# Kernel optimization log

Hardware: AMD Instinct MI355X
Metric: run time of the kernel (lower is better)

## Reference

```python
import jax, jax.numpy as jnp
import numpy as np

S, B, D, W = 2048, 4, 1024, 256  # seq_len, batch, d_model, local_window_size


def create_local_mask(seq_len, w):
    # Faithful to source: tril(w-1) then tril(-(w-1)) -> keeps j <= i-(w-1)
    m = jnp.ones((seq_len, seq_len), dtype=bool)
    m = jnp.tril(m, w - 1)
    m = jnp.tril(m, -(w - 1))
    return m


def setup_inputs() -> dict:
    key = jax.random.key(0)
    ks = jax.random.split(key, 12)
    w = lambda k: jax.random.normal(k, (D, D), dtype=jnp.float32) * 0.02
    return {
        "query": jax.random.normal(ks[0], (S, B, D), dtype=jnp.float32),
        "key_in": jax.random.normal(ks[1], (S, B, D), dtype=jnp.float32),
        "value": jax.random.normal(ks[2], (S, B, D), dtype=jnp.float32),
        "Wq": w(ks[3]), "bq": jnp.zeros((D,), jnp.float32),
        "Wk": w(ks[4]), "bk": jnp.zeros((D,), jnp.float32),
        "Wv": w(ks[5]), "bv": jnp.zeros((D,), jnp.float32),
        "pos_bias": jax.random.normal(ks[6], (S, S), dtype=jnp.float32) * 0.02,
        "Wo": w(ks[7]), "bo": jnp.zeros((D,), jnp.float32),
        "mask": jnp.ones((S, S, 1), dtype=bool),
    }


def reference(query, key_in, value, Wq, bq, Wk, bk, Wv, bv, pos_bias, Wo, bo, mask):
    # Linear projections (torch Linear: x @ W.T + b)
    q = jnp.einsum('sbd,ed->sbe', query, Wq) + bq
    k = jnp.einsum('sbd,ed->sbe', key_in, Wk) + bk
    v = jnp.einsum('sbd,ed->sbe', value, Wv) + bv

    local_mask = create_local_mask(S, W)
    pb = (pos_bias * local_mask.astype(pos_bias.dtype))[:, :, None]  # [S,S,1]
    pb = jnp.where(mask, pb, -jnp.inf)

    max_key = jnp.max(k, axis=0, keepdims=True)          # [1,B,D]
    max_pb = jnp.max(pb, axis=1, keepdims=True)          # [S,1,1]
    exp_key = jnp.exp(k - max_key)                       # [S,B,D]
    exp_pb = jnp.exp(pb - max_pb)                        # [S,S,B] after broadcast

    num = jnp.einsum('ijb,jbd->ibd', exp_pb, exp_key * v)
    den = jnp.einsum('ijb,jbd->ibd', exp_pb, exp_key)
    y = jax.nn.sigmoid(q) * num / den
    return jnp.einsum('sbd,ed->sbe', y, Wo) + bo
```

## Files before the change

kernel.cpp:

```cpp
#include <hip/hip_runtime.h>
#include <hip/hip_bf16.h>
#include <cstdint>


typedef short short8 __attribute__((ext_vector_type(8)));
typedef float f32x4 __attribute__((ext_vector_type(4)));

#define S_LEN 2048
#define NBD 4096
#define SBD 8388608
#define DD 1048576
#define SS 4194304

#define ASZ 8192
#define BUFSZ 24576
#define GASZ 4096
#define GBUF 12288
#define AS1 __attribute__((address_space(1)))
#define AS3 __attribute__((address_space(3)))

__device__ __forceinline__ unsigned short f2bf(float f) {
  union { float f; unsigned int u; } x; x.f = f;
  unsigned int u = x.u;
  unsigned int r = u + 0x7fffu + ((u >> 16) & 1u);
  return (unsigned short)(r >> 16);
}
__device__ __forceinline__ float bf2f(unsigned short b) {
  union { unsigned int u; float f; } x; x.u = ((unsigned int)b) << 16;
  return x.f;
}

__global__ __launch_bounds__(256) void k_cvt3(
    const float* __restrict__ a, const float* __restrict__ b, const float* __restrict__ c,
    unsigned short* __restrict__ oa, unsigned short* __restrict__ ob,
    unsigned short* __restrict__ oc) {
  const int w = blockIdx.x;
  const int arr = w >> 11;
  const int b2 = w & 2047;
  const float* src = arr == 0 ? a : (arr == 1 ? b : c);
  unsigned short* dst = arr == 0 ? oa : (arr == 1 ? ob : oc);
  const size_t t0 = (size_t)b2 * 256 + threadIdx.x;
#pragma unroll
  for (int it = 0; it < 2; ++it) {
    const size_t base = (t0 + (size_t)it * 524288) * 8;
    float4 x0 = *(const float4*)(src + base);
    float4 x1 = *(const float4*)(src + base + 4);
    short8 s;
    s[0] = (short)f2bf(x0.x); s[1] = (short)f2bf(x0.y);
    s[2] = (short)f2bf(x0.z); s[3] = (short)f2bf(x0.w);
    s[4] = (short)f2bf(x1.x); s[5] = (short)f2bf(x1.y);
    s[6] = (short)f2bf(x1.z); s[7] = (short)f2bf(x1.w);
    *(short8*)(dst + base) = s;
  }
}

__global__ void k_cvt4w(const float* __restrict__ wq, const float* __restrict__ wk,
                        const float* __restrict__ wv, const float* __restrict__ wo,
                        unsigned short* __restrict__ wcat, unsigned short* __restrict__ wob) {
  int i = (blockIdx.x * blockDim.x + threadIdx.x) * 4;
  float4 fq = *(const float4*)(wq + i);
  float4 fk = *(const float4*)(wk + i);
  float4 fv = *(const float4*)(wv + i);
  float4 fo = *(const float4*)(wo + i);
  ushort4 u;
  u.x = f2bf(fq.x); u.y = f2bf(fq.y); u.z = f2bf(fq.z); u.w = f2bf(fq.w);
  *(ushort4*)(wcat + i) = u;
  u.x = f2bf(fk.x); u.y = f2bf(fk.y); u.z = f2bf(fk.z); u.w = f2bf(fk.w);
  *(ushort4*)(wcat + DD + i) = u;
  u.x = f2bf(fv.x); u.y = f2bf(fv.y); u.z = f2bf(fv.z); u.w = f2bf(fv.w);
  *(ushort4*)(wcat + 2 * DD + i) = u;
  u.x = f2bf(fo.x); u.y = f2bf(fo.y); u.z = f2bf(fo.z); u.w = f2bf(fo.w);
  *(ushort4*)(wob + i) = u;
}

__global__ void k_build_c(const float* __restrict__ pb, unsigned short* __restrict__ C) {
  int i4 = (blockIdx.x * blockDim.x + threadIdx.x) * 4;
  float4 p = *(const float4*)(pb + i4);
  const int i = i4 >> 11;
  const int j = i4 & 2047;
  ushort4 o;
  o.x = f2bf((i >= j + 255) ? expm1f(p.x) : 0.0f);
  o.y = f2bf((i >= j + 256) ? expm1f(p.y) : 0.0f);
  o.z = f2bf((i >= j + 257) ? expm1f(p.z) : 0.0f);
  o.w = f2bf((i >= j + 258) ? expm1f(p.w) : 0.0f);
  *(ushort4*)(C + i4) = o;
}

__global__ __launch_bounds__(256) void k_eu_transpose(
    const unsigned short* __restrict__ kbf, const unsigned short* __restrict__ vbf,
    unsigned short* __restrict__ Mt, float* __restrict__ totals) {
  __shared__ unsigned short Lu[64][65];
  __shared__ unsigned short Le[64][65];
  const int n0 = blockIdx.x * 64;
  const int j0 = blockIdx.y * 64;
  const int t = threadIdx.x;
  const int c = t & 63;
  const int jq = t >> 6;
  float ptu = 0.f, pte = 0.f;
#pragma unroll 4
  for (int s = 0; s < 16; ++s) {
    int jj = jq + s * 4;
    size_t g = (size_t)(j0 + jj) * NBD + n0 + c;
    float kv = bf2f(kbf[g]);
    float vv = bf2f(vbf[g]);
    float e = __expf(kv);
    float u = e * vv;
    Le[jj][c] = f2bf(e);
    Lu[jj][c] = f2bf(u);
    pte += e; ptu += u;
  }
  atomicAdd(&totals[n0 + c], ptu);
  atomicAdd(&totals[NBD + n0 + c], pte);
  __syncthreads();
  const int jj2 = t & 63;
  const int nq = t >> 6;
#pragma unroll 4
  for (int s = 0; s < 16; ++s) {
    int nn = nq + s * 4;
    int ru = 2 * n0 + 32 * (nn >> 4) + (nn & 15);
    Mt[(size_t)ru * S_LEN + j0 + jj2] = Lu[jj2][nn];
    Mt[(size_t)(ru + 16) * S_LEN + j0 + jj2] = Le[jj2][nn];
  }
}

#define SBAR() do { __builtin_amdgcn_sched_barrier(0); __builtin_amdgcn_s_barrier(); \
                    __builtin_amdgcn_sched_barrier(0); } while (0)
#define VM(n)  do { asm volatile("s_waitcnt vmcnt(" #n ")" ::: "memory"); \
                    __builtin_amdgcn_sched_barrier(0); } while (0)
#define LGK0() do { asm volatile("s_waitcnt lgkmcnt(0)" ::: "memory"); \
                    __builtin_amdgcn_sched_barrier(0); } while (0)

#define G32_STAGE(tile, bidx) do {                                                        \
    const int k0_ = (tile) * 32;                                                          \
    __builtin_amdgcn_global_load_lds(                                                     \
        (const AS1 unsigned int*)(Ag + (size_t)(m0 + wave * 16 + lr4) * 1024 + k0_ + lc4),\
        (AS3 unsigned int*)&lds[(bidx) * GBUF + wave * 512 + lane * 8], 16, 0, 0);        \
    _Pragma("unroll") for (int q_ = 0; q_ < 2; ++q_) {                                    \
      const int g_ = wave * 2 + q_;                                                       \
      __builtin_amdgcn_global_load_lds(                                                   \
          (const AS1 unsigned int*)(Bg + (size_t)(n0 + g_ * 16 + lr4) * 1024 + k0_ + lc4),\
          (AS3 unsigned int*)&lds[(bidx) * GBUF + GASZ + g_ * 512 + lane * 8], 16, 0, 0); \
    }                                                                                     \
  } while (0)

#define G32_READF(RA, RB, bidx) do {                                                      \
    _Pragma("unroll") for (int f_ = 0; f_ < 4; ++f_)                                      \
      RA[f_] = *(const short8*)&lds[(bidx) * GBUF + (wr + f_ * 16 + l15) * 32 + swg];     \
    _Pragma("unroll") for (int f_ = 0; f_ < 4; ++f_)                                      \
      RB[f_] = *(const short8*)&lds[(bidx) * GBUF + GASZ + (wc + f_ * 16 + l15) * 32 + swg];\
  } while (0)

#define G32_MFMA(RA, RB) do {                                                             \
    __builtin_amdgcn_s_setprio(1);                                                        \
    _Pragma("unroll") for (int i_ = 0; i_ < 4; ++i_)                                      \
    _Pragma("unroll") for (int j_ = 0; j_ < 4; ++j_)                                      \
      acc[i_][j_] = __builtin_amdgcn_mfma_f32_16x16x32_bf16(RA[i_], RB[j_],               \
                                                            acc[i_][j_], 0, 0, 0);       \
    __builtin_amdgcn_s_setprio(0);                                                        \
  } while (0)

__global__ __launch_bounds__(512, 4) void k_qkv32(
    const unsigned short* __restrict__ A0, const unsigned short* __restrict__ A1,
    const unsigned short* __restrict__ A2, const unsigned short* __restrict__ Bg,
    const float* __restrict__ b0, const float* __restrict__ b1, const float* __restrict__ b2,
    unsigned short* __restrict__ o0, unsigned short* __restrict__ o1,
    unsigned short* __restrict__ o2) {
  __shared__ unsigned short lds[3 * GBUF];

  const int tid = threadIdx.x;
  const int wave = tid >> 6, lane = tid & 63;
  const int l15 = lane & 15, lh = lane >> 4;
  const int swg = (lh ^ ((l15 >> 1) & 3)) * 8;
  const int lr4 = lane >> 2;
  const int lc4 = ((lane & 3) ^ ((lane >> 3) & 3)) * 8;
  const int wr = (wave >> 2) * 64, wc = (wave & 3) * 64;

  const int w = blockIdx.x;
  const int xcd = w & 7, slot = w >> 3;
  const int mb = xcd * 8 + slot / 12;
  const int nb = slot % 12;
  const int m0 = mb * 128, n0 = nb * 256;
  const int grp = nb >> 2;
  const unsigned short* Ag = grp == 0 ? A0 : (grp == 1 ? A1 : A2);

  f32x4 acc[4][4];
#pragma unroll
  for (int i = 0; i < 4; ++i)
#pragma unroll
    for (int j = 0; j < 4; ++j)
      acc[i][j] = (f32x4){0.f, 0.f, 0.f, 0.f};

  short8 ra[4], rb[4];
  const int NT = 32;

  G32_STAGE(0, 0);
  G32_STAGE(1, 1);
  G32_STAGE(2, 2);
  VM(6);
  SBAR();
  G32_READF(ra, rb, 0);
  int cb = 0;
  for (int t = 0; t < NT; ++t) {
    G32_MFMA(ra, rb);
    if (t == NT - 1) break;
    LGK0();
    if (t + 2 <= NT - 1) VM(3); else VM(0);
    SBAR();
    int nbuf = cb + 1; if (nbuf == 3) nbuf = 0;
    G32_READF(ra, rb, nbuf);
    if (t + 3 <= NT - 1) G32_STAGE(t + 3, cb);
    cb = nbuf;
  }

  const float* bias = grp == 0 ? b0 : (grp == 1 ? b1 : b2);
  unsigned short* outp = grp == 0 ? o0 : (grp == 1 ? o1 : o2);
#pragma unroll
  for (int i = 0; i < 4; ++i)
#pragma unroll
    for (int j = 0; j < 4; ++j)
#pragma unroll
      for (int r = 0; r < 4; ++r) {
        const int row = m0 + wr + i * 16 + lh * 4 + r;
        const int col = (n0 + wc + j * 16 + l15) & 1023;
        float v = acc[i][j][r] + bias[col];
        if (grp == 0) v = 1.0f / (1.0f + __expf(-v));
        outp[(size_t)row * 1024 + col] = f2bf(v);
      }
}

#define STAGE(tile, bidx) do {                                                            \
    const int k0s_ = (tile) * 64;                                                         \
    _Pragma("unroll") for (int q_ = 0; q_ < 2; ++q_) {                                    \
      const int g_ = wave * 2 + q_;                                                       \
      __builtin_amdgcn_global_load_lds(                                                   \
          (const AS1 unsigned int*)(Ag + (size_t)(m0 + g_ * 8 + lr) * 2048 + k0s_ + lc),  \
          (AS3 unsigned int*)&lds[(bidx) * BUFSZ + g_ * 512], 16, 0, 0);                  \
    }                                                                                     \
    _Pragma("unroll") for (int q_ = 0; q_ < 4; ++q_) {                                    \
      const int g_ = wave * 4 + q_;                                                       \
      __builtin_amdgcn_global_load_lds(                                                   \
          (const AS1 unsigned int*)(Bg + (size_t)(n0 + g_ * 8 + lr) * 2048 + k0s_ + lc),  \
          (AS3 unsigned int*)&lds[(bidx) * BUFSZ + ASZ + g_ * 512], 16, 0, 0);            \
    }                                                                                     \
  } while (0)

#define READF(RA, RB, bidx, ks) do {                                                      \
    const int kof_ = (ks) * 32 + lh8;                                                     \
    _Pragma("unroll") for (int f_ = 0; f_ < 4; ++f_) {                                    \
      const int row_ = wr + f_ * 16 + l15;                                                \
      RA[f_] = *(const short8*)&lds[(bidx) * BUFSZ + row_ * 64 + (kof_ ^ swz)];           \
    }                                                                                     \
    _Pragma("unroll") for (int f_ = 0; f_ < 4; ++f_) {                                    \
      const int row_ = wc + f_ * 16 + l15;                                                \
      RB[f_] = *(const short8*)&lds[(bidx) * BUFSZ + ASZ + row_ * 64 + (kof_ ^ swz)];     \
    }                                                                                     \
  } while (0)

#define MFMA16(RA, RB) do {                                                               \
    __builtin_amdgcn_s_setprio(1);                                                        \
    _Pragma("unroll") for (int i_ = 0; i_ < 4; ++i_)                                      \
    _Pragma("unroll") for (int j_ = 0; j_ < 4; ++j_)                                      \
      acc[i_][j_] = __builtin_amdgcn_mfma_f32_16x16x32_bf16(RA[i_], RB[j_],               \
                                                            acc[i_][j_], 0, 0, 0);       \
    __builtin_amdgcn_s_setprio(0);                                                        \
  } while (0)

__global__ __launch_bounds__(512, 2) void k_tri(
    const unsigned short* __restrict__ Ag, const unsigned short* __restrict__ Bg,
    const float* __restrict__ totals, const unsigned short* __restrict__ sq,
    unsigned short* __restrict__ Y) {
  __shared__ unsigned short lds[3 * BUFSZ];

  const int tid = threadIdx.x;
  const int wave = tid >> 6, lane = tid & 63;
  const int l15 = lane & 15, lh = lane >> 4;
  const int lh8 = lh * 8;
  const int swz = (l15 & 7) * 8;
  const int lr = lane >> 3;
  const int lc = ((lane & 7) ^ lr) * 8;
  const int wr = (wave >> 2) * 64, wc = (wave & 3) * 64;

  const int w = blockIdx.x;
  const int mb = 15 - (w >> 5);
  const int nb = w & 31;
  const int m0 = mb * 128, n0 = nb * 256;
  const int NT = mb > 0 ? 2 * mb - 1 : 0;

  f32x4 acc[4][4];
#pragma unroll
  for (int i = 0; i < 4; ++i)
#pragma unroll
    for (int j = 0; j < 4; ++j)
      acc[i][j] = (f32x4){0.f, 0.f, 0.f, 0.f};

  short8 ra0[4], rb0[4], ra1[4], rb1[4];

  if (NT > 0) {
    STAGE(0, 0);
    if (NT > 1) STAGE(1, 1);
    if (NT > 2) STAGE(2, 2);
    if (NT > 2) VM(12); else if (NT > 1) VM(6); else VM(0);
    SBAR();
    READF(ra0, rb0, 0, 0);
    int cb = 0;
    for (int t = 0; t < NT; ++t) {
      READF(ra1, rb1, cb, 1);
      MFMA16(ra0, rb0);
      if (t < NT - 1) {
        LGK0();
        if (t + 2 <= NT - 1) VM(6); else VM(0);
        SBAR();
        int nbuf = cb + 1; if (nbuf == 3) nbuf = 0;
        READF(ra0, rb0, nbuf, 0);
        if (t + 3 <= NT - 1) STAGE(t + 3, cb);
        cb = nbuf;
        MFMA16(ra1, rb1);
      } else {
        MFMA16(ra1, rb1);
      }
    }
  }

#pragma unroll
  for (int i = 0; i < 4; ++i)
#pragma unroll
    for (int p = 0; p < 2; ++p) {
      const int n = ((n0 + wc) >> 1) + 16 * p + l15;
      const float tu = totals[n];
      const float te = totals[NBD + n];
#pragma unroll
      for (int r = 0; r < 4; ++r) {
        const int row = m0 + wr + i * 16 + lh * 4 + r;
        const size_t idx = (size_t)row * NBD + n;
        const float num = tu + acc[i][2 * p][r];
        const float den = te + acc[i][2 * p + 1][r];
        Y[idx] = f2bf(bf2f(sq[idx]) * num / den);
      }
    }
}

#define OSTAGE(tile, bidx) do {                                                           \
    const int k0s_ = (tile) * 64;                                                         \
    _Pragma("unroll") for (int q_ = 0; q_ < 2; ++q_) {                                    \
      const int g_ = wave * 2 + q_;                                                       \
      __builtin_amdgcn_global_load_lds(                                                   \
          (const AS1 unsigned int*)(Ag + (size_t)(m0 + g_ * 8 + lr) * 1024 + k0s_ + lc),  \
          (AS3 unsigned int*)&lds[(bidx) * BUFSZ + g_ * 512], 16, 0, 0);                  \
    }                                                                                     \
    _Pragma("unroll") for (int q_ = 0; q_ < 4; ++q_) {                                    \
      const int g_ = wave * 4 + q_;                                                       \
      __builtin_amdgcn_global_load_lds(                                                   \
          (const AS1 unsigned int*)(Bg + (size_t)(n0 + g_ * 8 + lr) * 1024 + k0s_ + lc),  \
          (AS3 unsigned int*)&lds[(bidx) * BUFSZ + ASZ + g_ * 512], 16, 0, 0);            \
    }                                                                                     \
  } while (0)

__global__ __launch_bounds__(512, 2) void k_gout(
    const unsigned short* __restrict__ Ag, const unsigned short* __restrict__ Bg,
    const float* __restrict__ bias, float* __restrict__ outp) {
  __shared__ unsigned short lds[3 * BUFSZ];

  const int tid = threadIdx.x;
  const int wave = tid >> 6, lane = tid & 63;
  const int l15 = lane & 15, lh = lane >> 4;
  const int lh8 = lh * 8;
  const int swz = (l15 & 7) * 8;
  const int lr = lane >> 3;
  const int lc = ((lane & 7) ^ lr) * 8;
  const int wr = (wave >> 2) * 64, wc = (wave & 3) * 64;

  const int w = blockIdx.x;
  const int xcd = w & 7, slot = w >> 3;
  const int mb = xcd * 8 + (slot >> 2), nb = slot & 3;
  const int m0 = mb * 128, n0 = nb * 256;

  f32x4 acc[4][4];
#pragma unroll
  for (int i = 0; i < 4; ++i)
#pragma unroll
    for (int j = 0; j < 4; ++j)
      acc[i][j] = (f32x4){0.f, 0.f, 0.f, 0.f};

  short8 ra0[4], rb0[4], ra1[4], rb1[4];

  OSTAGE(0, 0); OSTAGE(1, 1); OSTAGE(2, 2);
  VM(12);
  SBAR();
  READF(ra0, rb0, 0, 0);
  int cb = 0;
  const int NT = 16;
  for (int t = 0; t < NT; ++t) {
    READF(ra1, rb1, cb, 1);
    MFMA16(ra0, rb0);
    if (t < NT - 1) {
      LGK0();
      if (t + 2 <= NT - 1) VM(6); else VM(0);
      SBAR();
      int nbuf = cb + 1; if (nbuf == 3) nbuf = 0;
      READF(ra0, rb0, nbuf, 0);
      if (t + 3 <= NT - 1) OSTAGE(t + 3, cb);
      cb = nbuf;
    }
    MFMA16(ra1, rb1);
  }

#pragma unroll
  for (int i = 0; i < 4; ++i)
#pragma unroll
    for (int j = 0; j < 4; ++j)
#pragma unroll
      for (int r = 0; r < 4; ++r) {
        const int row = m0 + wr + i * 16 + lh * 4 + r;
        const int col = n0 + wc + j * 16 + l15;
        outp[(size_t)row * 1024 + col] = acc[i][j][r] + bias[col];
      }
}

extern "C" void kernel_launch(void* const* d_in, const int* in_sizes, int n_in,
                              void* d_out, int out_size, void* d_ws, size_t ws_size,
                              hipStream_t stream) {
  const float* query   = (const float*)d_in[0];
  const float* key_in  = (const float*)d_in[1];
  const float* value   = (const float*)d_in[2];
  const float* Wq      = (const float*)d_in[3];
  const float* bq      = (const float*)d_in[4];
  const float* Wk      = (const float*)d_in[5];
  const float* bk      = (const float*)d_in[6];
  const float* Wv      = (const float*)d_in[7];
  const float* bv      = (const float*)d_in[8];
  const float* pos_bias= (const float*)d_in[9];
  const float* Wo      = (const float*)d_in[10];
  const float* bo      = (const float*)d_in[11];
  float* out = (float*)d_out;

  char* wp = (char*)d_ws;
  auto alloc = [&](size_t bytes) -> char* {
    char* p = wp;
    wp += (bytes + 255) & ~(size_t)255;
    return p;
  };
  unsigned short* Xq   = (unsigned short*)alloc((size_t)SBD * 2);
  unsigned short* Xk   = (unsigned short*)alloc((size_t)SBD * 2);
  unsigned short* Xv   = (unsigned short*)alloc((size_t)SBD * 2);
  unsigned short* Wcat = (unsigned short*)alloc((size_t)3 * DD * 2);
  unsigned short* Wob  = (unsigned short*)alloc((size_t)DD * 2);
  unsigned short* Cb   = (unsigned short*)alloc((size_t)SS * 2);
  unsigned short* sigq = (unsigned short*)alloc((size_t)SBD * 2);
  unsigned short* kbf  = (unsigned short*)alloc((size_t)SBD * 2);
  unsigned short* vbf  = (unsigned short*)alloc((size_t)SBD * 2);
  unsigned short* Mt   = (unsigned short*)alloc((size_t)8192 * S_LEN * 2);
  float*          tot  = (float*)alloc((size_t)8192 * 4);
  unsigned short* Yb   = (unsigned short*)alloc((size_t)SBD * 2);

  k_cvt3<<<6144, 256, 0, stream>>>(query, key_in, value, Xq, Xk, Xv);
  k_cvt4w<<<DD / 4 / 256, 256, 0, stream>>>(Wq, Wk, Wv, Wo, Wcat, Wob);

  k_build_c<<<SS / 4 / 256, 256, 0, stream>>>(pos_bias, Cb);

  k_qkv32<<<768, 512, 0, stream>>>(Xq, Xk, Xv, Wcat, bq, bk, bv, sigq, kbf, vbf);

  hipMemsetAsync(tot, 0, 8192 * sizeof(float), stream);
  dim3 ge(NBD / 64, S_LEN / 64);
  k_eu_transpose<<<ge, 256, 0, stream>>>(kbf, vbf, Mt, tot);

  k_tri<<<512, 512, 0, stream>>>(Cb, Mt, tot, sigq, Yb);

  k_gout<<<256, 512, 0, stream>>>(Yb, Wob, bo, out);
}
```

Measured before the change: 181.9 us.

## Use K=32 tiles in triangular GEMM to halve LDS and raise occupancy

Replaces the triangular attention GEMM's K=64 staging with the smaller K=32 staging macro, parameterised by row stride, halving the shared-memory footprint so more blocks can reside per CU. Launch bounds are raised and the block-to-row-tile mapping is changed for the second half of the grid. Smaller K tiles mean more barriers and waits per unit of MFMA work, which may offset the occupancy gain.

Measured after the change: 178.5 us. Within noise of the previous version (-1.9%).

```diff
diff --git a/kernel.cpp b/kernel.cpp
--- a/kernel.cpp
+++ b/kernel.cpp
@@ -130,15 +130,15 @@
 #define LGK0() do { asm volatile("s_waitcnt lgkmcnt(0)" ::: "memory"); \
                     __builtin_amdgcn_sched_barrier(0); } while (0)
 
-#define G32_STAGE(tile, bidx) do {                                                        \
+#define G32_STAGE(tile, bidx, LD) do {                                                    \
     const int k0_ = (tile) * 32;                                                          \
     __builtin_amdgcn_global_load_lds(                                                     \
-        (const AS1 unsigned int*)(Ag + (size_t)(m0 + wave * 16 + lr4) * 1024 + k0_ + lc4),\
+        (const AS1 unsigned int*)(Ag + (size_t)(m0 + wave * 16 + lr4) * (LD) + k0_ + lc4),\
         (AS3 unsigned int*)&lds[(bidx) * GBUF + wave * 512 + lane * 8], 16, 0, 0);        \
     _Pragma("unroll") for (int q_ = 0; q_ < 2; ++q_) {                                    \
       const int g_ = wave * 2 + q_;                                                       \
       __builtin_amdgcn_global_load_lds(                                                   \
-          (const AS1 unsigned int*)(Bg + (size_t)(n0 + g_ * 16 + lr4) * 1024 + k0_ + lc4),\
+          (const AS1 unsigned int*)(Bg + (size_t)(n0 + g_ * 16 + lr4) * (LD) + k0_ + lc4),\
           (AS3 unsigned int*)&lds[(bidx) * GBUF + GASZ + g_ * 512 + lane * 8], 16, 0, 0); \
     }                                                                                     \
   } while (0)
@@ -193,9 +193,9 @@
   short8 ra[4], rb[4];
   const int NT = 32;
 
-  G32_STAGE(0, 0);
-  G32_STAGE(1, 1);
-  G32_STAGE(2, 2);
+  G32_STAGE(0, 0, 1024);
+  G32_STAGE(1, 1, 1024);
+  G32_STAGE(2, 2, 1024);
   VM(6);
   SBAR();
   G32_READF(ra, rb, 0);
@@ -208,7 +208,7 @@
     SBAR();
     int nbuf = cb + 1; if (nbuf == 3) nbuf = 0;
     G32_READF(ra, rb, nbuf);
-    if (t + 3 <= NT - 1) G32_STAGE(t + 3, cb);
+    if (t + 3 <= NT - 1) G32_STAGE(t + 3, cb, 1024);
     cb = nbuf;
   }
 
@@ -228,21 +228,73 @@
       }
 }
 
-#define STAGE(tile, bidx) do {                                                            \
-    const int k0s_ = (tile) * 64;                                                         \
-    _Pragma("unroll") for (int q_ = 0; q_ < 2; ++q_) {                                    \
-      const int g_ = wave * 2 + q_;                                                       \
-      __builtin_amdgcn_global_load_lds(                                                   \
-          (const AS1 unsigned int*)(Ag + (size_t)(m0 + g_ * 8 + lr) * 2048 + k0s_ + lc),  \
-          (AS3 unsigned int*)&lds[(bidx) * BUFSZ + g_ * 512], 16, 0, 0);                  \
-    }                                                                                     \
-    _Pragma("unroll") for (int q_ = 0; q_ < 4; ++q_) {                                    \
-      const int g_ = wave * 4 + q_;                                                       \
-      __builtin_amdgcn_global_load_lds(                                                   \
-          (const AS1 unsigned int*)(Bg + (size_t)(n0 + g_ * 8 + lr) * 2048 + k0s_ + lc),  \
-          (AS3 unsigned int*)&lds[(bidx) * BUFSZ + ASZ + g_ * 512], 16, 0, 0);            \
-    }                                                                                     \
-  } while (0)
+__global__ __launch_bounds__(512, 4) void k_tri32(
+    const unsigned short* __restrict__ Ag, const unsigned short* __restrict__ Bg,
+    const float* __restrict__ totals, const unsigned short* __restrict__ sq,
+    unsigned short* __restrict__ Y) {
+  __shared__ unsigned short lds[3 * GBUF];
+
+  const int tid = threadIdx.x;
+  const int wave = tid >> 6, lane = tid & 63;
+  const int l15 = lane & 15, lh = lane >> 4;
+  const int swg = (lh ^ ((l15 >> 1) & 3)) * 8;
+  const int lr4 = lane >> 2;
+  const int lc4 = ((lane & 3) ^ ((lane >> 3) & 3)) * 8;
+  const int wr = (wave >> 2) * 64, wc = (wave & 3) * 64;
+
+  const int w = blockIdx.x;
+  const int mb = (w < 256) ? (15 - (w >> 5)) : ((w - 256) >> 5);
+  const int nb = w & 31;
+  const int m0 = mb * 128, n0 = nb * 256;
+  const int NT = mb > 0 ? 4 * mb - 3 : 0;
+
+  f32x4 acc[4][4];
+#pragma unroll
+  for (int i = 0; i < 4; ++i)
+#pragma unroll
+    for (int j = 0; j < 4; ++j)
+      acc[i][j] = (f32x4){0.f, 0.f, 0.f, 0.f};
+
+  short8 ra[4], rb[4];
+
+  if (NT > 0) {
+    G32_STAGE(0, 0, 2048);
+    if (NT > 1) G32_STAGE(1, 1, 2048);
+    if (NT > 2) G32_STAGE(2, 2, 2048);
+    if (NT > 2) VM(6); else if (NT > 1) VM(3); else VM(0);
+    SBAR();
+    G32_READF(ra, rb, 0);
+    int cb = 0;
+    for (int t = 0; t < NT; ++t) {
+      G32_MFMA(ra, rb);
+      if (t == NT - 1) break;
+      LGK0();
+      if (t + 2 <= NT - 1) VM(3); else VM(0);
+      SBAR();
+      int nbuf = cb + 1; if (nbuf == 3) nbuf = 0;
+      G32_READF(ra, rb, nbuf);
+      if (t + 3 <= NT - 1) G32_STAGE(t + 3, cb, 2048);
+      cb = nbuf;
+    }
+  }
+
+#pragma unroll
+  for (int i = 0; i < 4; ++i)
+#pragma unroll
+    for (int p = 0; p < 2; ++p) {
+      const int n = ((n0 + wc) >> 1) + 16 * p + l15;
+      const float tu = totals[n];
+      const float te = totals[NBD + n];
+#pragma unroll
+      for (int r = 0; r < 4; ++r) {
+        const int row = m0 + wr + i * 16 + lh * 4 + r;
+        const size_t idx = (size_t)row * NBD + n;
+        const float num = tu + acc[i][2 * p][r];
+        const float den = te + acc[i][2 * p + 1][r];
+        Y[idx] = f2bf(bf2f(sq[idx]) * num / den);
+      }
+    }
+}
 
 #define READF(RA, RB, bidx, ks) do {                                                      \
     const int kof_ = (ks) * 32 + lh8;                                                     \
@@ -264,80 +316,6 @@
                                                             acc[i_][j_], 0, 0, 0);       \
     __builtin_amdgcn_s_setprio(0);                                                        \
   } while (0)
-
-__global__ __launch_bounds__(512, 2) void k_tri(
-    const unsigned short* __restrict__ Ag, const unsigned short* __restrict__ Bg,
-    const float* __restrict__ totals, const unsigned short* __restrict__ sq,
-    unsigned short* __restrict__ Y) {
-  __shared__ unsigned short lds[3 * BUFSZ];
-
-  const int tid = threadIdx.x;
-  const int wave = tid >> 6, lane = tid & 63;
-  const int l15 = lane & 15, lh = lane >> 4;
-  const int lh8 = lh * 8;
-  const int swz = (l15 & 7) * 8;
-  const int lr = lane >> 3;
-  const int lc = ((lane & 7) ^ lr) * 8;
-  const int wr = (wave >> 2) * 64, wc = (wave & 3) * 64;
-
-  const int w = blockIdx.x;
-  const int mb = 15 - (w >> 5);
-  const int nb = w & 31;
-  const int m0 = mb * 128, n0 = nb * 256;
-  const int NT = mb > 0 ? 2 * mb - 1 : 0;
-
-  f32x4 acc[4][4];
-#pragma unroll
-  for (int i = 0; i < 4; ++i)
-#pragma unroll
-    for (int j = 0; j < 4; ++j)
-      acc[i][j] = (f32x4){0.f, 0.f, 0.f, 0.f};
-
-  short8 ra0[4], rb0[4], ra1[4], rb1[4];
-
-  if (NT > 0) {
-    STAGE(0, 0);
-    if (NT > 1) STAGE(1, 1);
-    if (NT > 2) STAGE(2, 2);
-    if (NT > 2) VM(12); else if (NT > 1) VM(6); else VM(0);
-    SBAR();
-    READF(ra0, rb0, 0, 0);
-    int cb = 0;
-    for (int t = 0; t < NT; ++t) {
-      READF(ra1, rb1, cb, 1);
-      MFMA16(ra0, rb0);
-      if (t < NT - 1) {
-        LGK0();
-        if (t + 2 <= NT - 1) VM(6); else VM(0);
-        SBAR();
-        int nbuf = cb + 1; if (nbuf == 3) nbuf = 0;
-        READF(ra0, rb0, nbuf, 0);
-        if (t + 3 <= NT - 1) STAGE(t + 3, cb);
-        cb = nbuf;
-        MFMA16(ra1, rb1);
-      } else {
-        MFMA16(ra1, rb1);
-      }
-    }
-  }
-
-#pragma unroll
-  for (int i = 0; i < 4; ++i)
-#pragma unroll
-    for (int p = 0; p < 2; ++p) {
-      const int n = ((n0 + wc) >> 1) + 16 * p + l15;
-      const float tu = totals[n];
-      const float te = totals[NBD + n];
-#pragma unroll
-      for (int r = 0; r < 4; ++r) {
-        const int row = m0 + wr + i * 16 + lh * 4 + r;
-        const size_t idx = (size_t)row * NBD + n;
-        const float num = tu + acc[i][2 * p][r];
-        const float den = te + acc[i][2 * p + 1][r];
-        Y[idx] = f2bf(bf2f(sq[idx]) * num / den);
-      }
-    }
-}
 
 #define OSTAGE(tile, bidx) do {                                                           \
     const int k0s_ = (tile) * 64;                                                         \
@@ -463,7 +441,7 @@
   dim3 ge(NBD / 64, S_LEN / 64);
   k_eu_transpose<<<ge, 256, 0, stream>>>(kbf, vbf, Mt, tot);
 
-  k_tri<<<512, 512, 0, stream>>>(Cb, Mt, tot, sigq, Yb);
+  k_tri32<<<512, 512, 0, stream>>>(Cb, Mt, tot, sigq, Yb);
 
   k_gout<<<256, 512, 0, stream>>>(Yb, Wob, bo, out);
 }
```
